# Optimization experiments

Measured on AMD Instinct MI355X. Metric: run time of the kernel, lower is better.

The kernel has to match this reference:

```python
import jax, jax.numpy as jnp
import numpy as np

EMBED_DIM = 1024
NUM_HEADS = 16
D_K = EMBED_DIM // NUM_HEADS


def setup_inputs() -> dict:
    key = jax.random.key(0)
    ks = jax.random.split(key, 9)
    s = 1.0 / np.sqrt(EMBED_DIM)
    x = jax.random.normal(ks[0], (4, 2048, EMBED_DIM), dtype=jnp.float32)
    # nn.Linear weights stored as [out, in]; we keep [in, out] for x @ W
    W_q = jax.random.uniform(ks[1], (EMBED_DIM, EMBED_DIM), jnp.float32, -s, s)
    b_q = jax.random.uniform(ks[2], (EMBED_DIM,), jnp.float32, -s, s)
    W_k = jax.random.uniform(ks[3], (EMBED_DIM, EMBED_DIM), jnp.float32, -s, s)
    b_k = jax.random.uniform(ks[4], (EMBED_DIM,), jnp.float32, -s, s)
    W_v = jax.random.uniform(ks[5], (EMBED_DIM, EMBED_DIM), jnp.float32, -s, s)
    b_v = jax.random.uniform(ks[6], (EMBED_DIM,), jnp.float32, -s, s)
    W_o = jax.random.uniform(ks[7], (EMBED_DIM, EMBED_DIM), jnp.float32, -s, s)
    b_o = jax.random.uniform(ks[8], (EMBED_DIM,), jnp.float32, -s, s)
    return {"x": x, "W_q": W_q, "b_q": b_q, "W_k": W_k, "b_k": b_k,
            "W_v": W_v, "b_v": b_v, "W_o": W_o, "b_o": b_o}


def reference(x, W_q, b_q, W_k, b_k, W_v, b_v, W_o, b_o):
    B, N, _ = x.shape
    # QKV projections, split into heads: [B, H, N, d_k]
    def proj(W, b):
        return (x @ W + b).reshape(B, N, NUM_HEADS, D_K).transpose(0, 2, 1, 3)
    Q, K, V = proj(W_q, b_q), proj(W_k, b_k), proj(W_v, b_v)
    scale = 1.0 / np.sqrt(D_K).astype(np.float32)
    scores = jnp.einsum('bhqd,bhkd->bhqk', Q, K) * scale  # [B,H,N,N]
    weights = jax.nn.softmax(scores, axis=-1)
    # dropout is identity in eval mode
    attn = jnp.einsum('bhqk,bhkd->bhqd', weights, V)  # [B,H,N,d_k]
    attn = attn.transpose(0, 2, 1, 3).reshape(B, N, EMBED_DIM)
    return attn @ W_o + b_o
```

## Files before the change

kernel.cpp:

```cpp
#include <hip/hip_runtime.h>

typedef __bf16 bf16;
typedef __attribute__((ext_vector_type(8))) __bf16 bf16x8;
typedef __attribute__((ext_vector_type(4))) __bf16 bf16x4;
typedef __attribute__((ext_vector_type(4))) float f32x4;

static __device__ __forceinline__ f32x4 mfma16(bf16x8 a, bf16x8 b, f32x4 c) {
    return __builtin_amdgcn_mfma_f32_16x16x32_bf16(a, b, c, 0, 0, 0);
}

static __device__ __forceinline__ void gll16(const bf16* g, bf16* l) {
    __builtin_amdgcn_global_load_lds(
        (const __attribute__((address_space(1))) unsigned int*)g,
        (__attribute__((address_space(3))) unsigned int*)l, 16, 0, 0);
}

__global__ __launch_bounds__(256) void xcvt_kernel(
    const float* __restrict__ x, bf16* __restrict__ xb)
{
    size_t i = ((size_t)blockIdx.x * 256 + threadIdx.x) * 8;
    float4 a0 = *(const float4*)&x[i];
    float4 a1 = *(const float4*)&x[i + 4];
    bf16x8 v = {(bf16)a0.x, (bf16)a0.y, (bf16)a0.z, (bf16)a0.w,
                (bf16)a1.x, (bf16)a1.y, (bf16)a1.z, (bf16)a1.w};
    *(bf16x8*)&xb[i] = v;
}

__global__ __launch_bounds__(256) void wtrans_kernel(
    const float* __restrict__ Wq, const float* __restrict__ Wk,
    const float* __restrict__ Wv, const float* __restrict__ Wo,
    bf16* __restrict__ WTqkv, bf16* __restrict__ WTo)
{
    __shared__ bf16 tile[64][65];
    const int bid = blockIdx.x;
    const int mi = bid >> 8;
    const int t  = bid & 255;
    const int tr = t >> 4;
    const int tc = t & 15;
    const int tid = threadIdx.x;

    const float* src = (mi == 0) ? Wq : (mi == 1) ? Wk : (mi == 2) ? Wv : Wo;
    bf16* dst = (mi < 3) ? (WTqkv + (size_t)mi * 1024 * 1024) : WTo;

    #pragma unroll
    for (int i = 0; i < 16; i++) {
        int idx = i * 256 + tid;
        int rl = idx >> 6, cl = idx & 63;
        tile[rl][cl] = (bf16)src[(size_t)(tr * 64 + rl) * 1024 + tc * 64 + cl];
    }
    __syncthreads();
    #pragma unroll
    for (int i = 0; i < 16; i++) {
        int idx = i * 256 + tid;
        int rl = idx >> 6, cl = idx & 63;
        dst[(size_t)(tc * 64 + rl) * 1024 + tr * 64 + cl] = tile[cl][rl];
    }
}

__global__ void biascat_kernel(const float* __restrict__ bq, const float* __restrict__ bk,
                               const float* __restrict__ bv, float* __restrict__ dst)
{
    int i = blockIdx.x * 256 + threadIdx.x;
    if (i < 1024) dst[i] = bq[i];
    else if (i < 2048) dst[i] = bk[i - 1024];
    else dst[i] = bv[i - 2048];
}

#define QSCALE 0.18033688011112043f
__global__ __launch_bounds__(256) void gemm_bf16_kernel(
    const bf16* __restrict__ A, const bf16* __restrict__ BT,
    const float* __restrict__ bias, bf16* __restrict__ C,
    int M, int N, int K, int scaleQ)
{
    __shared__ bf16 sA[128 * 32];
    __shared__ bf16 sB[128 * 32];
    const int tid  = threadIdx.x;
    const int lane = tid & 63;
    const int wave = tid >> 6;
    const int quad = lane >> 4;
    const int l15  = lane & 15;
    const int wm = (wave >> 1) * 64;
    const int wn = (wave & 1) * 64;
    const int m0 = blockIdx.y * 128;
    const int n0 = blockIdx.x * 128;

    const f32x4 fzero = {0.f, 0.f, 0.f, 0.f};
    f32x4 acc[4][4];
    #pragma unroll
    for (int i = 0; i < 4; i++)
        #pragma unroll
        for (int j = 0; j < 4; j++) acc[i][j] = fzero;

    float bv[4];
    #pragma unroll
    for (int nc = 0; nc < 4; nc++) bv[nc] = bias[n0 + wn + nc * 16 + l15];

    const int rA = lane >> 2;
    const int cA = (lane & 3) * 8;

    for (int k0 = 0; k0 < K; k0 += 32) {
        #pragma unroll
        for (int p = 0; p < 2; p++) {
            int r16 = (wave * 2 + p) * 16;
            gll16(&A[(size_t)(m0 + r16 + rA) * K + k0 + cA], &sA[r16 * 32]);
            gll16(&BT[(size_t)(n0 + r16 + rA) * K + k0 + cA], &sB[r16 * 32]);
        }
        __syncthreads();

        bf16x8 aF[4], bF[4];
        #pragma unroll
        for (int mc = 0; mc < 4; mc++)
            aF[mc] = *(const bf16x8*)&sA[(wm + mc * 16 + l15) * 32 + quad * 8];
        #pragma unroll
        for (int nc = 0; nc < 4; nc++)
            bF[nc] = *(const bf16x8*)&sB[(wn + nc * 16 + l15) * 32 + quad * 8];

        #pragma unroll
        for (int mc = 0; mc < 4; mc++)
            #pragma unroll
            for (int nc = 0; nc < 4; nc++)
                acc[mc][nc] = mfma16(aF[mc], bF[nc], acc[mc][nc]);
        __syncthreads();
    }

    const float sc = (scaleQ && n0 < 1024) ? QSCALE : 1.0f;
    #pragma unroll
    for (int mc = 0; mc < 4; mc++) {
        #pragma unroll
        for (int reg = 0; reg < 4; reg++) {
            int row = m0 + wm + mc * 16 + quad * 4 + reg;
            size_t base = (size_t)row * N + n0 + wn;
            #pragma unroll
            for (int nc = 0; nc < 4; nc++)
                C[base + nc * 16 + l15] = (bf16)((acc[mc][nc][reg] + bv[nc]) * sc);
        }
    }
}

__global__ __launch_bounds__(256) void gemm_bf16_f32out_kernel(
    const bf16* __restrict__ A, const bf16* __restrict__ BT,
    const float* __restrict__ bias, float* __restrict__ C,
    int M, int N, int K)
{
    __shared__ bf16 sA[128 * 32];
    __shared__ bf16 sB[128 * 32];
    const int tid  = threadIdx.x;
    const int lane = tid & 63;
    const int wave = tid >> 6;
    const int quad = lane >> 4;
    const int l15  = lane & 15;
    const int wm = (wave >> 1) * 64;
    const int wn = (wave & 1) * 64;
    const int m0 = blockIdx.y * 128;
    const int n0 = blockIdx.x * 128;

    const f32x4 fzero = {0.f, 0.f, 0.f, 0.f};
    f32x4 acc[4][4];
    #pragma unroll
    for (int i = 0; i < 4; i++)
        #pragma unroll
        for (int j = 0; j < 4; j++) acc[i][j] = fzero;

    float bv[4];
    #pragma unroll
    for (int nc = 0; nc < 4; nc++) bv[nc] = bias[n0 + wn + nc * 16 + l15];

    const int rA = lane >> 2;
    const int cA = (lane & 3) * 8;

    for (int k0 = 0; k0 < K; k0 += 32) {
        #pragma unroll
        for (int p = 0; p < 2; p++) {
            int r16 = (wave * 2 + p) * 16;
            gll16(&A[(size_t)(m0 + r16 + rA) * K + k0 + cA], &sA[r16 * 32]);
            gll16(&BT[(size_t)(n0 + r16 + rA) * K + k0 + cA], &sB[r16 * 32]);
        }
        __syncthreads();

        bf16x8 aF[4], bF[4];
        #pragma unroll
        for (int mc = 0; mc < 4; mc++)
            aF[mc] = *(const bf16x8*)&sA[(wm + mc * 16 + l15) * 32 + quad * 8];
        #pragma unroll
        for (int nc = 0; nc < 4; nc++)
            bF[nc] = *(const bf16x8*)&sB[(wn + nc * 16 + l15) * 32 + quad * 8];

        #pragma unroll
        for (int mc = 0; mc < 4; mc++)
            #pragma unroll
            for (int nc = 0; nc < 4; nc++)
                acc[mc][nc] = mfma16(aF[mc], bF[nc], acc[mc][nc]);
        __syncthreads();
    }

    #pragma unroll
    for (int mc = 0; mc < 4; mc++) {
        #pragma unroll
        for (int reg = 0; reg < 4; reg++) {
            int row = m0 + wm + mc * 16 + quad * 4 + reg;
            size_t base = (size_t)row * N + n0 + wn;
            #pragma unroll
            for (int nc = 0; nc < 4; nc++)
                C[base + nc * 16 + l15] = acc[mc][nc][reg] + bv[nc];
        }
    }
}

__global__ __launch_bounds__(256) void vtrans_kernel(
    const bf16* __restrict__ QKVp, bf16* __restrict__ Vt)
{
    __shared__ bf16 tile[64][65];
    const int bid = blockIdx.x;
    const int bh = bid >> 5;
    const int nt = bid & 31;
    const int b = bh >> 4, h = bh & 15;
    const int tid = threadIdx.x;

    #pragma unroll
    for (int i = 0; i < 16; i++) {
        int idx = i * 256 + tid;
        int rl = idx >> 6, cl = idx & 63;
        tile[rl][cl] = QKVp[(size_t)(b * 2048 + nt * 64 + rl) * 3072 + 2048 + h * 64 + cl];
    }
    __syncthreads();
    #pragma unroll
    for (int i = 0; i < 16; i++) {
        int idx = i * 256 + tid;
        int rl = idx >> 6, cl = idx & 63;
        Vt[((size_t)bh * 64 + rl) * 2048 + nt * 64 + cl] = tile[cl][rl];
    }
}

__global__ __launch_bounds__(256) void attn_kernel(
    const bf16* __restrict__ QKV, const bf16* __restrict__ Vt,
    bf16* __restrict__ Opre)
{
    __shared__ bf16 sK[2][64 * 64];
    __shared__ bf16 sV[2][64 * 64];

    const int tid  = threadIdx.x;
    const int lane = tid & 63;
    const int w    = tid >> 6;
    const int quad = lane >> 4;
    const int l15  = lane & 15;
    const int bid = blockIdx.x;
    const int bh = bid >> 4;
    const int qt = bid & 15;
    const int b = bh >> 4, h = bh & 15;
    const int q0 = qt * 128;

    bf16x8 qF[2][2];
    #pragma unroll
    for (int g = 0; g < 2; g++) {
        size_t qrow = (size_t)(b * 2048 + q0 + w * 32 + g * 16 + l15) * 3072 + h * 64;
        qF[g][0] = *(const bf16x8*)&QKV[qrow + quad * 8];
        qF[g][1] = *(const bf16x8*)&QKV[qrow + 32 + quad * 8];
    }

    const f32x4 fzero = {0.f, 0.f, 0.f, 0.f};
    float psum[2] = {0.f, 0.f};
    f32x4 o[2][4];
    #pragma unroll
    for (int g = 0; g < 2; g++)
        #pragma unroll
        for (int mt = 0; mt < 4; mt++) o[g][mt] = fzero;

    const int srow = tid >> 3, sseg = tid & 7;
    const size_t kbase = (size_t)(b * 2048) * 3072 + 1024 + h * 64;
    const size_t vbase = (size_t)bh * 64 * 2048;
    const int sgsw = sseg ^ ((srow & 3) | (((srow >> 3) & 1) << 2));

    const int swk = (l15 & 3) | (((l15 >> 2) & 1) << 2);
    const int swv = (l15 & 3) | (((l15 >> 3) & 1) << 2);

    bf16x8 stK[2], stV[2];

    #pragma unroll
    for (int p = 0; p < 2; p++) {
        int row = srow + p * 32;
        stK[p] = *(const bf16x8*)&QKV[kbase + (size_t)row * 3072 + sseg * 8];
        stV[p] = *(const bf16x8*)&Vt[vbase + (size_t)row * 2048 + sseg * 8];
    }
    #pragma unroll
    for (int p = 0; p < 2; p++) {
        int row = srow + p * 32;
        *(bf16x8*)&sK[0][row * 64 + sgsw * 8] = stK[p];
        *(bf16x8*)&sV[0][row * 64 + sgsw * 8] = stV[p];
    }
    __syncthreads();

    auto compute_tile = [&](const bf16* sKc, const bf16* sVc) {
        bf16x8 pB[2][2];
        #pragma unroll
        for (int c = 0; c < 4; c++) {
            int kr = ((l15 >> 2) << 3) + ((c & 1) << 2) + (l15 & 3) + ((c >> 1) << 5);
            bf16x8 kA0 = *(const bf16x8*)&sKc[kr * 64 + ((quad ^ swk) * 8)];
            bf16x8 kA1 = *(const bf16x8*)&sKc[kr * 64 + (((4 + quad) ^ swk) * 8)];
            #pragma unroll
            for (int g = 0; g < 2; g++) {
                __builtin_amdgcn_s_setprio(1);
                f32x4 st = mfma16(kA0, qF[g][0], fzero);
                st = mfma16(kA1, qF[g][1], st);
                __builtin_amdgcn_s_setprio(0);
                #pragma unroll
                for (int r = 0; r < 4; r++) {
                    float p = __builtin_amdgcn_exp2f(st[r]);
                    psum[g] += p;
                    pB[g][c >> 1][(c & 1) * 4 + r] = (bf16)p;
                }
            }
        }
        #pragma unroll
        for (int mt = 0; mt < 4; mt++) {
            int vr = mt * 16 + l15;
            bf16x8 vA0 = *(const bf16x8*)&sVc[vr * 64 + ((quad ^ swv) * 8)];
            bf16x8 vA1 = *(const bf16x8*)&sVc[vr * 64 + (((4 + quad) ^ swv) * 8)];
            __builtin_amdgcn_s_setprio(1);
            #pragma unroll
            for (int g = 0; g < 2; g++) {
                o[g][mt] = mfma16(vA0, pB[g][0], o[g][mt]);
                o[g][mt] = mfma16(vA1, pB[g][1], o[g][mt]);
            }
            __builtin_amdgcn_s_setprio(0);
        }
    };

    int cur = 0;
    for (int t = 0; t < 31; t++) {
        const int key0 = (t + 1) * 64;
        #pragma unroll
        for (int p = 0; p < 2; p++) {
            int row = srow + p * 32;
            stK[p] = *(const bf16x8*)&QKV[kbase + (size_t)(key0 + row) * 3072 + sseg * 8];
            stV[p] = *(const bf16x8*)&Vt[vbase + (size_t)row * 2048 + key0 + sseg * 8];
        }
        __builtin_amdgcn_sched_barrier(0);

        compute_tile(sK[cur], sV[cur]);

        #pragma unroll
        for (int p = 0; p < 2; p++) {
            int row = srow + p * 32;
            *(bf16x8*)&sK[cur ^ 1][row * 64 + sgsw * 8] = stK[p];
            *(bf16x8*)&sV[cur ^ 1][row * 64 + sgsw * 8] = stV[p];
        }
        __syncthreads();
        cur ^= 1;
    }
    compute_tile(sK[cur], sV[cur]);

    #pragma unroll
    for (int g = 0; g < 2; g++) {
        float t = psum[g];
        t += __shfl_xor(t, 16);
        t += __shfl_xor(t, 32);
        float inv = 1.0f / t;
        size_t obase = (size_t)(b * 2048 + q0 + w * 32 + g * 16 + l15) * 1024 + h * 64;
        #pragma unroll
        for (int mt = 0; mt < 4; mt++) {
            bf16x4 ov = {(bf16)(o[g][mt][0] * inv), (bf16)(o[g][mt][1] * inv),
                         (bf16)(o[g][mt][2] * inv), (bf16)(o[g][mt][3] * inv)};
            *(bf16x4*)&Opre[obase + mt * 16 + quad * 4] = ov;
        }
    }
}

extern "C" void kernel_launch(void* const* d_in, const int* in_sizes, int n_in,
                              void* d_out, int out_size, void* d_ws, size_t ws_size,
                              hipStream_t stream)
{
    const float* x  = (const float*)d_in[0];
    const float* Wq = (const float*)d_in[1];
    const float* bq = (const float*)d_in[2];
    const float* Wk = (const float*)d_in[3];
    const float* bk = (const float*)d_in[4];
    const float* Wv = (const float*)d_in[5];
    const float* bv = (const float*)d_in[6];
    const float* Wo = (const float*)d_in[7];
    const float* bo = (const float*)d_in[8];
    float* out = (float*)d_out;

    bf16* WTqkv = (bf16*)d_ws;
    bf16* WTo   = WTqkv + (size_t)3072 * 1024;
    float* bcat = (float*)(WTo + (size_t)1024 * 1024);
    bf16* QKVp  = (bf16*)(bcat + 4096);
    bf16* Vt    = QKVp + (size_t)8192 * 3072;
    bf16* Apre  = Vt + (size_t)64 * 64 * 2048;
    bf16* xb    = Apre;
    (void)ws_size; (void)n_in; (void)in_sizes; (void)out_size;

    xcvt_kernel<<<4096, 256, 0, stream>>>(x, xb);
    wtrans_kernel<<<1024, 256, 0, stream>>>(Wq, Wk, Wv, Wo, WTqkv, WTo);
    biascat_kernel<<<12, 256, 0, stream>>>(bq, bk, bv, bcat);
    gemm_bf16_kernel<<<dim3(24, 64), 256, 0, stream>>>(xb, WTqkv, bcat, QKVp, 8192, 3072, 1024, 1);
    vtrans_kernel<<<2048, 256, 0, stream>>>(QKVp, Vt);
    attn_kernel<<<1024, 256, 0, stream>>>(QKVp, Vt, Apre);
    gemm_bf16_f32out_kernel<<<dim3(8, 64), 256, 0, stream>>>(Apre, WTo, bo, out, 8192, 1024, 1024);
}
```

Measured before the change: 299.3 us.

## Prefetch two KV tiles ahead, compute row sums with MFMA, remap block order

The attention loop now holds two register staging sets, so global loads for tile t+2 are in flight while tile t is computed, giving a deeper prefetch than the single-tile lookahead. The per-lane scalar softmax denominator accumulation and the final cross-lane shuffles are replaced by an MFMA against a ones vector on the bf16 probabilities, which moves that work to the matrix unit. The sum is now taken over bf16-rounded values, so it matches the values used in the P·V product. Block indices are also permuted so that consecutive workgroups are spread across heads and batches, changing L2 locality per XCD. The extra staging registers may raise register pressure and lower occupancy.

```diff
diff --git a/kernel.cpp b/kernel.cpp
--- a/kernel.cpp
+++ b/kernel.cpp
@@ -243,7 +243,7 @@
     const int w    = tid >> 6;
     const int quad = lane >> 4;
     const int l15  = lane & 15;
-    const int bid = blockIdx.x;
+    const int bid = (blockIdx.x & 7) * 128 + (blockIdx.x >> 3);
     const int bh = bid >> 4;
     const int qt = bid & 15;
     const int b = bh >> 4, h = bh & 15;
@@ -258,7 +258,9 @@
     }
 
     const f32x4 fzero = {0.f, 0.f, 0.f, 0.f};
-    float psum[2] = {0.f, 0.f};
+    const bf16 one = (bf16)1.0f;
+    const bf16x8 ones = {one, one, one, one, one, one, one, one};
+    f32x4 ps[2] = {fzero, fzero};
     f32x4 o[2][4];
     #pragma unroll
     for (int g = 0; g < 2; g++)
@@ -273,21 +275,23 @@
     const int swk = (l15 & 3) | (((l15 >> 2) & 1) << 2);
     const int swv = (l15 & 3) | (((l15 >> 3) & 1) << 2);
 
-    bf16x8 stK[2], stV[2];
-
-    #pragma unroll
-    for (int p = 0; p < 2; p++) {
-        int row = srow + p * 32;
-        stK[p] = *(const bf16x8*)&QKV[kbase + (size_t)row * 3072 + sseg * 8];
-        stV[p] = *(const bf16x8*)&Vt[vbase + (size_t)row * 2048 + sseg * 8];
-    }
-    #pragma unroll
-    for (int p = 0; p < 2; p++) {
-        int row = srow + p * 32;
-        *(bf16x8*)&sK[0][row * 64 + sgsw * 8] = stK[p];
-        *(bf16x8*)&sV[0][row * 64 + sgsw * 8] = stV[p];
-    }
-    __syncthreads();
+    bf16x8 stAK[2], stAV[2], stBK[2], stBV[2];
+
+#define ISSUE(RK, RV, KEY0)                                                       \
+    _Pragma("unroll")                                                             \
+    for (int p = 0; p < 2; p++) {                                                 \
+        int row = srow + p * 32;                                                  \
+        RK[p] = *(const bf16x8*)&QKV[kbase + (size_t)((KEY0) + row) * 3072 + sseg * 8]; \
+        RV[p] = *(const bf16x8*)&Vt[vbase + (size_t)row * 2048 + (KEY0) + sseg * 8];    \
+    }
+
+#define COMMIT(RK, RV, BUF)                                                       \
+    _Pragma("unroll")                                                             \
+    for (int p = 0; p < 2; p++) {                                                 \
+        int row = srow + p * 32;                                                  \
+        *(bf16x8*)&sK[BUF][row * 64 + sgsw * 8] = RK[p];                          \
+        *(bf16x8*)&sV[BUF][row * 64 + sgsw * 8] = RV[p];                          \
+    }
 
     auto compute_tile = [&](const bf16* sKc, const bf16* sVc) {
         bf16x8 pB[2][2];
@@ -305,11 +309,17 @@
                 #pragma unroll
                 for (int r = 0; r < 4; r++) {
                     float p = __builtin_amdgcn_exp2f(st[r]);
-                    psum[g] += p;
                     pB[g][c >> 1][(c & 1) * 4 + r] = (bf16)p;
                 }
             }
         }
+        __builtin_amdgcn_s_setprio(1);
+        #pragma unroll
+        for (int g = 0; g < 2; g++) {
+            ps[g] = mfma16(ones, pB[g][0], ps[g]);
+            ps[g] = mfma16(ones, pB[g][1], ps[g]);
+        }
+        __builtin_amdgcn_s_setprio(0);
         #pragma unroll
         for (int mt = 0; mt < 4; mt++) {
             int vr = mt * 16 + l15;
@@ -325,36 +335,35 @@
         }
     };
 
-    int cur = 0;
-    for (int t = 0; t < 31; t++) {
-        const int key0 = (t + 1) * 64;
-        #pragma unroll
-        for (int p = 0; p < 2; p++) {
-            int row = srow + p * 32;
-            stK[p] = *(const bf16x8*)&QKV[kbase + (size_t)(key0 + row) * 3072 + sseg * 8];
-            stV[p] = *(const bf16x8*)&Vt[vbase + (size_t)row * 2048 + key0 + sseg * 8];
-        }
+    ISSUE(stAK, stAV, 0);
+    ISSUE(stBK, stBV, 64);
+    COMMIT(stAK, stAV, 0);
+    __syncthreads();
+
+    for (int t = 0; t < 30; t += 2) {
+        ISSUE(stAK, stAV, (t + 2) * 64);
         __builtin_amdgcn_sched_barrier(0);
-
-        compute_tile(sK[cur], sV[cur]);
-
-        #pragma unroll
-        for (int p = 0; p < 2; p++) {
-            int row = srow + p * 32;
-            *(bf16x8*)&sK[cur ^ 1][row * 64 + sgsw * 8] = stK[p];
-            *(bf16x8*)&sV[cur ^ 1][row * 64 + sgsw * 8] = stV[p];
-        }
-        __syncthreads();
-        cur ^= 1;
-    }
-    compute_tile(sK[cur], sV[cur]);
+        compute_tile(sK[0], sV[0]);
+        COMMIT(stBK, stBV, 1);
+        __syncthreads();
+
+        ISSUE(stBK, stBV, (t + 3) * 64);
+        __builtin_amdgcn_sched_barrier(0);
+        compute_tile(sK[1], sV[1]);
+        COMMIT(stAK, stAV, 0);
+        __syncthreads();
+    }
+    compute_tile(sK[0], sV[0]);
+    COMMIT(stBK, stBV, 1);
+    __syncthreads();
+    compute_tile(sK[1], sV[1]);
+
+#undef ISSUE
+#undef COMMIT
 
     #pragma unroll
     for (int g = 0; g < 2; g++) {
-        float t = psum[g];
-        t += __shfl_xor(t, 16);
-        t += __shfl_xor(t, 32);
-        float inv = 1.0f / t;
+        float inv = 1.0f / ps[g][0];
         size_t obase = (size_t)(b * 2048 + q0 + w * 32 + g * 16 + l15) * 1024 + h * 64;
         #pragma unroll
         for (int mt = 0; mt < 4; mt++) {
```

Measured after the change: 299.8 us. No clear change (+0.2%).
